# Optimization experiments

Measured on AMD Instinct MI355X. Metric: run time of the kernel, lower is better.

Reference implementation:

```python
import jax, jax.numpy as jnp
import numpy as np

EMBED = 64
TEMPERATURE = 8.0
LN_EPS = 1e-6


def setup_inputs() -> dict:
    key = jax.random.key(0)
    ks = jax.random.split(key, 9)
    n_map, n_obs = 16384, 8192
    s = 1.0 / np.sqrt(EMBED)
    return {
        "map_code": jax.random.normal(ks[0], (n_map, EMBED), jnp.float32),
        "obs_code": jax.random.normal(ks[1], (n_obs, EMBED), jnp.float32),
        "Wq": jax.random.normal(ks[2], (EMBED, EMBED), jnp.float32) * s,
        "Wk": jax.random.normal(ks[3], (EMBED, EMBED), jnp.float32) * s,
        "Wv": jax.random.normal(ks[4], (EMBED, EMBED), jnp.float32) * s,
        "Wo": jax.random.normal(ks[5], (EMBED // 2, EMBED), jnp.float32) * (1.0 / np.sqrt(EMBED // 2)),
        "bo": jnp.zeros((EMBED,), jnp.float32),
        "gamma": jnp.ones((EMBED,), jnp.float32),
        "beta": jnp.zeros((EMBED,), jnp.float32),
    }


def _glu(x):
    a, b = jnp.split(x, 2, axis=-1)
    return a * jax.nn.sigmoid(b)


def reference(map_code, obs_code, Wq, Wk, Wv, Wo, bo, gamma, beta):
    # projections (x @ W == torch Linear with weight W.T; params are random either way)
    map_q = map_code @ Wq          # [Nm, E]
    map_k = map_code @ Wk          # [Nm, E]
    map_v = map_code @ Wv          # [Nm, E]
    obs_k = obs_code @ Wk          # [No, E]
    obs_v = obs_code @ Wv          # [No, E]

    self_score = jnp.sum(map_q * map_k, axis=-1, keepdims=True)   # [Nm, 1]
    obs_score = map_q @ obs_k.T                                   # [Nm, No]
    w = jax.nn.softmax(
        jnp.concatenate([self_score, obs_score], axis=-1) / TEMPERATURE,
        axis=-1,
    )  # [Nm, 1+No]

    # GLU gating: glu(obs_v) is identical for every map row, so the original's
    # [Nm, 1+No, E] broadcast collapses to a rank-2 contraction.
    gated_map = _glu(map_v)   # [Nm, E/2]
    gated_obs = _glu(obs_v)   # [No, E/2]
    agg = w[:, :1] * gated_map + w[:, 1:] @ gated_obs   # [Nm, E/2]

    out = agg @ Wo + bo + map_code   # [Nm, E]
    mu = jnp.mean(out, axis=-1, keepdims=True)
    var = jnp.mean(jnp.square(out - mu), axis=-1, keepdims=True)
    return (out - mu) * jax.lax.rsqrt(var + LN_EPS) * gamma + beta
```

## Files before the change

### kernel.cpp

```cpp
#include <hip/hip_runtime.h>
#include <hip/hip_bf16.h>


typedef float f32x16 __attribute__((ext_vector_type(16)));
typedef short bf16x8 __attribute__((ext_vector_type(8)));
typedef unsigned int u32;

__device__ __forceinline__ u32 cvt_pk_bf16(float lo, float hi) {
    u32 r;
    asm("v_cvt_pk_bf16_f32 %0, %1, %2" : "=v"(r) : "v"(lo), "v"(hi));
    return r;
}
__device__ __forceinline__ void permswap32(u32& a, u32& b) {
    asm("v_permlane32_swap_b32 %0, %1" : "+v"(a), "+v"(b));
}

#define IT 0.18033688011112042f
#define LOG2E 1.44269504089f

__global__ __launch_bounds__(256) void prep_kernel(
    const float* __restrict__ map_code, const float* __restrict__ obs_code,
    const float* __restrict__ Wq, const float* __restrict__ Wk,
    const float* __restrict__ Wv,
    __hip_bfloat16* __restrict__ qbf, __hip_bfloat16* __restrict__ Kp,
    __hip_bfloat16* __restrict__ Vp, float* __restrict__ self_score,
    float* __restrict__ gated_map, int n_map, int n_obs)
{
    __shared__ float xs[32 * 64];
    const int t = threadIdx.x;
    const int w = t >> 6;
    const int e = t & 63;
    const int r0 = blockIdx.x * 32;
    const int total = n_map + n_obs;

    #pragma unroll
    for (int i = 0; i < 8; ++i) {
        const int idx = i * 256 + t;
        const int gr = r0 + (idx >> 6);
        const int col = idx & 63;
        float val = 0.0f;
        if (gr < n_map)      val = map_code[(size_t)gr * 64 + col];
        else if (gr < total) val = obs_code[(size_t)(gr - n_map) * 64 + col];
        xs[idx] = val;
    }
    __syncthreads();

    float qa[8] = {}, ka[8] = {}, va[8] = {};
    const float* xw = xs + (w * 8) * 64;
    #pragma unroll 4
    for (int d = 0; d < 64; ++d) {
        const float wq = Wq[d * 64 + e];
        const float wk = Wk[d * 64 + e];
        const float wv = Wv[d * 64 + e];
        #pragma unroll
        for (int i = 0; i < 8; ++i) {
            const float x = xw[i * 64 + d];
            qa[i] = fmaf(x, wq, qa[i]);
            ka[i] = fmaf(x, wk, ka[i]);
            va[i] = fmaf(x, wv, va[i]);
        }
    }

    #pragma unroll
    for (int i = 0; i < 8; ++i) {
        const int r = r0 + w * 8 + i;
        if (r >= total) break;
        const bool is_map = r < n_map;
        const float vother = __shfl_xor(va[i], 32);
        const float sig = 1.0f / (1.0f + __builtin_amdgcn_exp2f(-vother * LOG2E));
        const float g = va[i] * sig;

        if (is_map) {
            qbf[(size_t)r * 64 + e] = __float2bfloat16(qa[i] * IT);
            float qk = qa[i] * ka[i];
            #pragma unroll
            for (int off = 32; off; off >>= 1) qk += __shfl_xor(qk, off);
            if (e == 0) self_score[r] = qk;
            if (e < 32) gated_map[(size_t)r * 32 + e] = g;
        } else {
            const int j  = r - n_map;
            const int kb = j >> 5, jq = j & 31;
            {
                const int c = e >> 4, h2 = (e >> 3) & 1, ii = e & 7;
                Kp[(size_t)kb * 2048 + c * 512 + (h2 * 32 + jq) * 8 + ii] =
                    __float2bfloat16(ka[i]);
            }
            if (e < 32) {
                const int h = jq >> 4, h3 = (jq >> 3) & 1, ii = jq & 7;
                Vp[(size_t)kb * 1024 + h * 512 + (h3 * 32 + e) * 8 + ii] =
                    __float2bfloat16(g);
            }
        }
    }
}

#define WAVES 4
__global__ __launch_bounds__(64 * WAVES, 4) void attn_partial(
    const __hip_bfloat16* __restrict__ qbf, const __hip_bfloat16* __restrict__ Kp,
    const __hip_bfloat16* __restrict__ Vp,
    __hip_bfloat16* __restrict__ oP, float* __restrict__ lP,
    int n_obs, int n_map, int kslog)
{
    const int tid  = threadIdx.x;
    const int w    = tid >> 6;
    const int lane = tid & 63;
    const int ql   = lane & 31;
    const int hi   = lane >> 5;
    const int ks   = 1 << kslog;
    const int qb   = blockIdx.x >> kslog;
    const int slice= blockIdx.x & (ks - 1);
    const int tileT= qb * WAVES + w;
    const int q    = tileT * 32 + ql;

    __shared__ __align__(16) char kv[2][12288];

    bf16x8 qf[4];
    {
        const __hip_bfloat16* qrow = qbf + (size_t)q * 64 + 8 * hi;
        #pragma unroll
        for (int c = 0; c < 4; ++c)
            qf[c] = *reinterpret_cast<const bf16x8*>(qrow + c * 16);
    }

    float lsumA = 0.0f, lsumB = 0.0f;
    f32x16 o = {};

    const int nkb      = (n_obs >> kslog) >> 5;
    const int kb_begin = slice * nkb;
    const int npairs   = nkb >> 1;
    const char* Kb = (const char*)Kp;
    const char* Vb = (const char*)Vp;

    uint4 gK0, gK1, gV;
    auto gloadPair = [&](int kb0) {
        const char* ksrc = Kb + (size_t)kb0 * 4096 + tid * 32;
        gK0 = *reinterpret_cast<const uint4*>(ksrc);
        gK1 = *reinterpret_cast<const uint4*>(ksrc + 16);
        gV  = *reinterpret_cast<const uint4*>(Vb + (size_t)kb0 * 2048 + tid * 16);
    };
    auto swritePair = [&](char* buf) {
        *reinterpret_cast<uint4*>(buf + tid * 32)        = gK0;
        *reinterpret_cast<uint4*>(buf + tid * 32 + 16)   = gK1;
        *reinterpret_cast<uint4*>(buf + 8192 + tid * 16) = gV;
    };
    auto readsub = [&](const char* buf, int j, bf16x8 (&kf)[4], bf16x8 (&vf)[2]) {
        const char* kbp = buf + j * 4096 + lane * 16;
        #pragma unroll
        for (int c = 0; c < 4; ++c)
            kf[c] = *reinterpret_cast<const bf16x8*>(kbp + c * 1024);
        const char* vbp = buf + 8192 + j * 2048 + lane * 16;
        vf[0] = *reinterpret_cast<const bf16x8*>(vbp);
        vf[1] = *reinterpret_cast<const bf16x8*>(vbp + 1024);
    };

    auto body = [&](const bf16x8 (&kf)[4], const bf16x8 (&vf)[2]) {
        f32x16 s = {};
        #pragma unroll
        for (int c = 0; c < 4; ++c)
            s = __builtin_amdgcn_mfma_f32_32x32x16_bf16(kf[c], qf[c], s, 0, 0, 0);
        float p[16];
        #pragma unroll
        for (int r = 0; r < 16; ++r) p[r] = __builtin_amdgcn_exp2f(s[r]);
        #pragma unroll
        for (int r = 0; r < 8; ++r) { lsumA += p[r]; lsumB += p[r + 8]; }
        union { u32 u[4]; bf16x8 v; } pb0, pb1;
        {
            u32 x0 = cvt_pk_bf16(p[0], p[1]);
            u32 x1 = cvt_pk_bf16(p[2], p[3]);
            u32 y0 = cvt_pk_bf16(p[4], p[5]);
            u32 y1 = cvt_pk_bf16(p[6], p[7]);
            permswap32(x0, y0);
            permswap32(x1, y1);
            pb0.u[0] = x0; pb0.u[1] = x1; pb0.u[2] = y0; pb0.u[3] = y1;
        }
        {
            u32 x0 = cvt_pk_bf16(p[8],  p[9]);
            u32 x1 = cvt_pk_bf16(p[10], p[11]);
            u32 y0 = cvt_pk_bf16(p[12], p[13]);
            u32 y1 = cvt_pk_bf16(p[14], p[15]);
            permswap32(x0, y0);
            permswap32(x1, y1);
            pb1.u[0] = x0; pb1.u[1] = x1; pb1.u[2] = y0; pb1.u[3] = y1;
        }
        o = __builtin_amdgcn_mfma_f32_32x32x16_bf16(vf[0], pb0.v, o, 0, 0, 0);
        o = __builtin_amdgcn_mfma_f32_32x32x16_bf16(vf[1], pb1.v, o, 0, 0, 0);
    };

    gloadPair(kb_begin);
    swritePair(kv[0]);
    gloadPair(npairs > 1 ? kb_begin + 2 : kb_begin);

    int cur = 0;
    bf16x8 kf[4], vf[2];
    for (int r = 0; r < npairs; ++r) {
        __syncthreads();
        readsub(kv[cur], 0, kf, vf);
        swritePair(kv[cur ^ 1]);
        gloadPair(r + 2 < npairs ? kb_begin + 2 * (r + 2) : kb_begin);
        body(kf, vf);
        readsub(kv[cur], 1, kf, vf);
        body(kf, vf);
        cur ^= 1;
    }

    float lsum = lsumA + lsumB;
    lsum += __shfl_xor(lsum, 32);
    if (hi == 0) lP[(size_t)slice * n_map + tileT * 32 + ql] = lsum;
    __hip_bfloat16* ob = oP + ((size_t)slice * (n_map >> 5) + tileT) * 1024;
    #pragma unroll
    for (int r = 0; r < 16; ++r) {
        const int vr = (r & 3) + 8 * (r >> 2) + 4 * hi;
        ob[vr * 32 + ql] = __float2bfloat16(o[r]);
    }
}

__global__ __launch_bounds__(256) void combine_epi(
    const __hip_bfloat16* __restrict__ oP, const float* __restrict__ lP,
    const float* __restrict__ self_score, const float* __restrict__ gated_map,
    const float* __restrict__ map_code, const float* __restrict__ Wo,
    const float* __restrict__ bo, const float* __restrict__ gamma,
    const float* __restrict__ beta, float* __restrict__ out,
    int n_map, int ks)
{
    const int tid  = threadIdx.x;
    const int w    = tid >> 6;
    const int lane = tid & 63;
    const int T    = blockIdx.x;
    const int q0   = T * 32;
    const int ntiles = n_map >> 5;

    __shared__ float aggT[32][33];
    __shared__ float invS[32];
    __shared__ float psS[32];

    if (tid < 32) {
        const float ps = __builtin_amdgcn_exp2f(self_score[q0 + tid] * IT);
        psS[tid] = ps;
        float l = ps;
        for (int s = 0; s < ks; ++s)
            l += lP[(size_t)s * n_map + q0 + tid];
        invS[tid] = 1.0f / l;
    }
    __syncthreads();

    #pragma unroll
    for (int t = tid; t < 1024; t += 256) {
        const int v  = t >> 5;
        const int qq = t & 31;
        float a = psS[qq] * gated_map[(size_t)(q0 + qq) * 32 + v];
        for (int s = 0; s < ks; ++s)
            a += __bfloat162float(oP[((size_t)s * ntiles + T) * 1024 + t]);
        aggT[v][qq] = a;
    }
    __syncthreads();

    float wo[32];
    #pragma unroll
    for (int vv = 0; vv < 32; ++vv) wo[vv] = Wo[vv * 64 + lane];
    const float bo_e = bo[lane], ga = gamma[lane], be = beta[lane];

    #pragma unroll
    for (int i = 0; i < 8; ++i) {
        const int qq = w * 8 + i;
        float dot = 0.0f;
        #pragma unroll
        for (int vv = 0; vv < 32; ++vv)
            dot = fmaf(aggT[vv][qq], wo[vv], dot);
        float acc = dot * invS[qq] + bo_e + map_code[(size_t)(q0 + qq) * 64 + lane];
        float mu = acc;
        #pragma unroll
        for (int off = 32; off; off >>= 1) mu += __shfl_xor(mu, off);
        mu *= (1.0f / 64.0f);
        const float dc = acc - mu;
        float var = dc * dc;
        #pragma unroll
        for (int off = 32; off; off >>= 1) var += __shfl_xor(var, off);
        var *= (1.0f / 64.0f);
        out[(size_t)(q0 + qq) * 64 + lane] =
            dc * rsqrtf(var + 1e-6f) * ga + be;
    }
}

extern "C" void kernel_launch(void* const* d_in, const int* in_sizes, int n_in,
                              void* d_out, int out_size, void* d_ws, size_t ws_size,
                              hipStream_t stream) {
    const float* map_code = (const float*)d_in[0];
    const float* obs_code = (const float*)d_in[1];
    const float* Wq  = (const float*)d_in[2];
    const float* Wk  = (const float*)d_in[3];
    const float* Wv  = (const float*)d_in[4];
    const float* Wo  = (const float*)d_in[5];
    const float* bo  = (const float*)d_in[6];
    const float* gam = (const float*)d_in[7];
    const float* bet = (const float*)d_in[8];
    const int n_map = in_sizes[0] / 64;
    const int n_obs = in_sizes[1] / 64;
    const int ntiles = n_map / 32;

    char* ws = (char*)d_ws;
    __hip_bfloat16* qbf = (__hip_bfloat16*)ws; ws += (size_t)n_map * 64 * 2;
    __hip_bfloat16* Kp  = (__hip_bfloat16*)ws; ws += (size_t)n_obs * 64 * 2;
    __hip_bfloat16* Vp  = (__hip_bfloat16*)ws; ws += (size_t)n_obs * 32 * 2;
    float* self_score   = (float*)ws;          ws += (size_t)n_map * 4;
    float* gated_map    = (float*)ws;          ws += (size_t)n_map * 32 * 4;
    const size_t base   = (size_t)(ws - (char*)d_ws);
    const size_t per_slice = (size_t)n_map * 32 * 2 + (size_t)n_map * 4;
    int kslog = 3;
    while (kslog > 0 && base + ((size_t)1 << kslog) * per_slice > ws_size)
        --kslog;
    const int ks = 1 << kslog;
    __hip_bfloat16* oP = (__hip_bfloat16*)ws; ws += (size_t)ks * n_map * 32 * 2;
    float* lP = (float*)ws;

    const int total = n_map + n_obs;
    prep_kernel<<<(total + 31) / 32, 256, 0, stream>>>(
        map_code, obs_code, Wq, Wk, Wv, qbf, Kp, Vp, self_score, gated_map,
        n_map, n_obs);
    attn_partial<<<(n_map / 128) * ks, 64 * WAVES, 0, stream>>>(
        qbf, Kp, Vp, oP, lP, n_obs, n_map, kslog);
    combine_epi<<<ntiles, 256, 0, stream>>>(
        oP, lP, self_score, gated_map, map_code, Wo, bo, gam, bet,
        (float*)d_out, n_map, ks);
}
```

Baseline: 70.60 us.

## Process two query tiles per wave to reuse K/V fragments, double key splits

```diff
diff --git a/kernel.cpp b/kernel.cpp
--- a/kernel.cpp
+++ b/kernel.cpp
@@ -109,21 +109,26 @@
     const int ks   = 1 << kslog;
     const int qb   = blockIdx.x >> kslog;
     const int slice= blockIdx.x & (ks - 1);
-    const int tileT= qb * WAVES + w;
-    const int q    = tileT * 32 + ql;
+    const int tile1= qb * 8 + w;
+    const int tile2= tile1 + 4;
+    const int q1   = tile1 * 32 + ql;
+    const int q2   = tile2 * 32 + ql;
 
     __shared__ __align__(16) char kv[2][12288];
 
-    bf16x8 qf[4];
+    bf16x8 qf1[4], qf2[4];
     {
-        const __hip_bfloat16* qrow = qbf + (size_t)q * 64 + 8 * hi;
-        #pragma unroll
-        for (int c = 0; c < 4; ++c)
-            qf[c] = *reinterpret_cast<const bf16x8*>(qrow + c * 16);
-    }
-
-    float lsumA = 0.0f, lsumB = 0.0f;
-    f32x16 o = {};
+        const __hip_bfloat16* qrow1 = qbf + (size_t)q1 * 64 + 8 * hi;
+        const __hip_bfloat16* qrow2 = qbf + (size_t)q2 * 64 + 8 * hi;
+        #pragma unroll
+        for (int c = 0; c < 4; ++c) {
+            qf1[c] = *reinterpret_cast<const bf16x8*>(qrow1 + c * 16);
+            qf2[c] = *reinterpret_cast<const bf16x8*>(qrow2 + c * 16);
+        }
+    }
+
+    float l1A = 0.0f, l1B = 0.0f, l2A = 0.0f, l2B = 0.0f;
+    f32x16 o1 = {}, o2 = {};
 
     const int nkb      = (n_obs >> kslog) >> 5;
     const int kb_begin = slice * nkb;
@@ -153,16 +158,17 @@
         vf[1] = *reinterpret_cast<const bf16x8*>(vbp + 1024);
     };
 
-    auto body = [&](const bf16x8 (&kf)[4], const bf16x8 (&vf)[2]) {
+    auto bodyT = [&](const bf16x8 (&qft)[4], f32x16& ot, float& lA, float& lB,
+                     const bf16x8 (&kf)[4], const bf16x8 (&vf)[2]) {
         f32x16 s = {};
         #pragma unroll
         for (int c = 0; c < 4; ++c)
-            s = __builtin_amdgcn_mfma_f32_32x32x16_bf16(kf[c], qf[c], s, 0, 0, 0);
+            s = __builtin_amdgcn_mfma_f32_32x32x16_bf16(kf[c], qft[c], s, 0, 0, 0);
         float p[16];
         #pragma unroll
         for (int r = 0; r < 16; ++r) p[r] = __builtin_amdgcn_exp2f(s[r]);
         #pragma unroll
-        for (int r = 0; r < 8; ++r) { lsumA += p[r]; lsumB += p[r + 8]; }
+        for (int r = 0; r < 8; ++r) { lA += p[r]; lB += p[r + 8]; }
         union { u32 u[4]; bf16x8 v; } pb0, pb1;
         {
             u32 x0 = cvt_pk_bf16(p[0], p[1]);
@@ -182,8 +188,8 @@
             permswap32(x1, y1);
             pb1.u[0] = x0; pb1.u[1] = x1; pb1.u[2] = y0; pb1.u[3] = y1;
         }
-        o = __builtin_amdgcn_mfma_f32_32x32x16_bf16(vf[0], pb0.v, o, 0, 0, 0);
-        o = __builtin_amdgcn_mfma_f32_32x32x16_bf16(vf[1], pb1.v, o, 0, 0, 0);
+        ot = __builtin_amdgcn_mfma_f32_32x32x16_bf16(vf[0], pb0.v, ot, 0, 0, 0);
+        ot = __builtin_amdgcn_mfma_f32_32x32x16_bf16(vf[1], pb1.v, ot, 0, 0, 0);
     };
 
     gloadPair(kb_begin);
@@ -197,20 +203,28 @@
         readsub(kv[cur], 0, kf, vf);
         swritePair(kv[cur ^ 1]);
         gloadPair(r + 2 < npairs ? kb_begin + 2 * (r + 2) : kb_begin);
-        body(kf, vf);
+        bodyT(qf1, o1, l1A, l1B, kf, vf);
+        bodyT(qf2, o2, l2A, l2B, kf, vf);
         readsub(kv[cur], 1, kf, vf);
-        body(kf, vf);
+        bodyT(qf1, o1, l1A, l1B, kf, vf);
+        bodyT(qf2, o2, l2A, l2B, kf, vf);
         cur ^= 1;
     }
 
-    float lsum = lsumA + lsumB;
-    lsum += __shfl_xor(lsum, 32);
-    if (hi == 0) lP[(size_t)slice * n_map + tileT * 32 + ql] = lsum;
-    __hip_bfloat16* ob = oP + ((size_t)slice * (n_map >> 5) + tileT) * 1024;
+    float l1 = l1A + l1B, l2 = l2A + l2B;
+    l1 += __shfl_xor(l1, 32);
+    l2 += __shfl_xor(l2, 32);
+    if (hi == 0) {
+        lP[(size_t)slice * n_map + tile1 * 32 + ql] = l1;
+        lP[(size_t)slice * n_map + tile2 * 32 + ql] = l2;
+    }
+    __hip_bfloat16* ob1 = oP + ((size_t)slice * (n_map >> 5) + tile1) * 1024;
+    __hip_bfloat16* ob2 = oP + ((size_t)slice * (n_map >> 5) + tile2) * 1024;
     #pragma unroll
     for (int r = 0; r < 16; ++r) {
         const int vr = (r & 3) + 8 * (r >> 2) + 4 * hi;
-        ob[vr * 32 + ql] = __float2bfloat16(o[r]);
+        ob1[vr * 32 + ql] = __float2bfloat16(o1[r]);
+        ob2[vr * 32 + ql] = __float2bfloat16(o2[r]);
     }
 }
 
@@ -305,7 +319,7 @@
     float* gated_map    = (float*)ws;          ws += (size_t)n_map * 32 * 4;
     const size_t base   = (size_t)(ws - (char*)d_ws);
     const size_t per_slice = (size_t)n_map * 32 * 2 + (size_t)n_map * 4;
-    int kslog = 3;
+    int kslog = 4;
     while (kslog > 0 && base + ((size_t)1 << kslog) * per_slice > ws_size)
         --kslog;
     const int ks = 1 << kslog;
@@ -316,7 +330,7 @@
     prep_kernel<<<(total + 31) / 32, 256, 0, stream>>>(
         map_code, obs_code, Wq, Wk, Wv, qbf, Kp, Vp, self_score, gated_map,
         n_map, n_obs);
-    attn_partial<<<(n_map / 128) * ks, 64 * WAVES, 0, stream>>>(
+    attn_partial<<<(n_map / 256) * ks, 64 * WAVES, 0, stream>>>(
         qbf, Kp, Vp, oP, lP, n_obs, n_map, kslog);
     combine_epi<<<ntiles, 256, 0, stream>>>(
         oP, lP, self_score, gated_map, map_code, Wo, bo, gam, bet,
```

Result: slower. 117.5 us (+66.5%).
